# Kernel optimization log

Hardware: AMD Instinct MI355X
Metric: run time of the kernel (lower is better)

The kernel has to match this reference:

```python
import jax, jax.numpy as jnp
import numpy as np

B, S_SRC, S_TGT = 4096, 32, 32
V_SRC, V_TGT, E, H = 96, 128, 128, 512
SOS = 1


def _lstm_cell(h, c, x, Wih, Whh, bih, bhh):
    # PyTorch LSTM gate layout: [i, f, g, o] along 4H
    gates = x @ Wih.T + bih + h @ Whh.T + bhh  # (B, 4H)
    i, f, g, o = jnp.split(gates, 4, axis=-1)
    i, f, o = jax.nn.sigmoid(i), jax.nn.sigmoid(f), jax.nn.sigmoid(o)
    g = jnp.tanh(g)
    c2 = f * c + i * g
    h2 = o * jnp.tanh(c2)
    return h2, c2


def setup_inputs() -> dict:
    key = jax.random.key(0)
    ks = jax.random.split(key, 16)
    u = lambda k, shp, s: jax.random.uniform(k, shp, jnp.float32, -s, s)
    sh = 1.0 / np.sqrt(H)
    emb_src = u(ks[0], (V_SRC, E), 0.1).at[0].set(0.0)  # padding_idx=0
    emb_tgt = u(ks[1], (V_TGT, E), 0.1).at[0].set(0.0)
    inp = {
        "src_seq": jax.random.randint(ks[2], (B, S_SRC), 1, V_SRC),
        "src_lengths": jax.random.randint(ks[3], (B,), 1, S_SRC + 1),
        "tgt_seq": jax.random.randint(ks[4], (B, S_TGT), 1, V_TGT),
        "emb_src": emb_src,
        "enc_Wih": u(ks[5], (4 * H, E), sh),
        "enc_Whh": u(ks[6], (4 * H, H), sh),
        "enc_bih": u(ks[7], (4 * H,), sh),
        "enc_bhh": u(ks[8], (4 * H,), sh),
        "emb_tgt": emb_tgt,
        "dec_Wih": u(ks[9], (4 * H, E), sh),
        "dec_Whh": u(ks[10], (4 * H, H), sh),
        "dec_bih": u(ks[11], (4 * H,), sh),
        "dec_bhh": u(ks[12], (4 * H,), sh),
        "W_out": u(ks[13], (V_TGT, H), sh),
        "b_out": u(ks[14], (V_TGT,), sh),
    }
    return inp


def reference(src_seq, src_lengths, tgt_seq,
              emb_src, enc_Wih, enc_Whh, enc_bih, enc_bhh,
              emb_tgt, dec_Wih, dec_Whh, dec_bih, dec_bhh,
              W_out, b_out):
    batch = src_seq.shape[0]
    h0 = jnp.zeros((batch, H), jnp.float32)
    c0 = jnp.zeros((batch, H), jnp.float32)

    # ---- Encoder: masked LSTM == pack_padded_sequence semantics ----
    x_src = emb_src[src_seq]                                # (B, S, E)
    x_src_t = jnp.swapaxes(x_src, 0, 1)                     # (S, B, E)
    mask = (jnp.arange(S_SRC)[:, None] < src_lengths[None, :])[:, :, None]  # (S,B,1)

    def enc_step(carry, inp):
        h, c = carry
        x, m = inp
        h2, c2 = _lstm_cell(h, c, x, enc_Wih, enc_Whh, enc_bih, enc_bhh)
        h = jnp.where(m, h2, h)
        c = jnp.where(m, c2, c)
        return (h, c), None

    (h_enc, c_enc), _ = jax.lax.scan(enc_step, (h0, c0), (x_src_t, mask))

    # ---- Decoder: full teacher forcing (ratio=1.0), eval-mode dropout ----
    dec_in = jnp.concatenate(
        [jnp.full((batch, 1), SOS, tgt_seq.dtype), tgt_seq[:, :-1]], axis=1)  # (B, T)
    x_tgt_t = jnp.swapaxes(emb_tgt[dec_in], 0, 1)           # (T, B, E)

    def dec_step(carry, x):
        h, c = carry
        h2, c2 = _lstm_cell(h, c, x, dec_Wih, dec_Whh, dec_bih, dec_bhh)
        return (h2, c2), h2

    _, hs = jax.lax.scan(dec_step, (h_enc, c_enc), x_tgt_t)  # (T, B, H)

    logits = jnp.einsum('tbh,vh->btv', hs, W_out) + b_out    # (B, T, V_TGT)
    return logits
```

## Files before the change

### kernel.cpp

```cpp
#include <hip/hip_runtime.h>
#include <hip/hip_bf16.h>
#include <hip/hip_fp16.h>
#include <stdint.h>


#define NB     4096
#define SSRC   32
#define STGT   32
#define NVSRC  96
#define NVTGT  128
#define ED     128
#define HD     512
#define G4     2048
#define NBHD   ((size_t)NB * HD)

typedef __attribute__((ext_vector_type(8))) _Float16 half8;
typedef __attribute__((ext_vector_type(4))) float fx4;

#define AS_G __attribute__((address_space(1)))
#define AS_L __attribute__((address_space(3)))

__device__ __forceinline__ void gl2lds16(const void* g, void* l) {
    __builtin_amdgcn_global_load_lds((const AS_G uint32_t*)g, (AS_L uint32_t*)l, 16, 0, 0);
}

__device__ __forceinline__ float sigf(float x) { return 1.0f / (1.0f + __expf(-x)); }
__device__ __forceinline__ float tanhfast(float x) { return 1.0f - 2.0f / (__expf(2.0f * x) + 1.0f); }

__global__ __launch_bounds__(256) void convert_all(
    const float* __restrict__ s1, int n1, _Float16* __restrict__ d1,
    const float* __restrict__ s2, int n2, _Float16* __restrict__ d2,
    const float* __restrict__ s3, int n3, _Float16* __restrict__ d3)
{
    int i = (int)blockIdx.x * 256 + threadIdx.x;
    if (i < n1) { d1[i] = (_Float16)s1[i]; return; }
    i -= n1;
    if (i < n2) { d2[i] = (_Float16)s2[i]; return; }
    i -= n2;
    if (i < n3) d3[i] = (_Float16)s3[i];
}

__global__ __launch_bounds__(256) void transpose2_f32(
    const float* __restrict__ inA, float* __restrict__ outTA,
    const float* __restrict__ inB, float* __restrict__ outTB)
{
    __shared__ float ls[32][33];
    int bid = (int)blockIdx.x;
    const float* in; float* outT;
    if (bid < 256) { in = inA; outT = outTA; }
    else           { in = inB; outT = outTB; bid -= 256; }
    const int rtiles = G4 / 32;
    const int bx = bid % rtiles;
    const int by = bid / rtiles;
    const int tx = threadIdx.x & 31, ty = threadIdx.x >> 5;
    #pragma unroll
    for (int i = 0; i < 4; i++) {
        int rr = ty + i * 8;
        ls[rr][tx] = in[(size_t)(bx * 32 + rr) * ED + by * 32 + tx];
    }
    __syncthreads();
    #pragma unroll
    for (int i = 0; i < 4; i++) {
        int rr = ty + i * 8;
        outT[(size_t)(by * 32 + rr) * G4 + bx * 32 + tx] = ls[tx][rr];
    }
}

__global__ __launch_bounds__(256) void build_tables2(
    const float* __restrict__ embS, const float* __restrict__ WTS,
    const float* __restrict__ bihS, const float* __restrict__ bhhS,
    float* __restrict__ projS,
    const float* __restrict__ embT, const float* __restrict__ WTT,
    const float* __restrict__ bihT, const float* __restrict__ bhhT,
    float* __restrict__ projT)
{
    __shared__ float embL[8][ED];
    int bid = (int)blockIdx.x;
    const float *emb, *WT, *bih, *bhh; float* proj;
    if (bid < (NVSRC / 8) * 8) { emb = embS; WT = WTS; bih = bihS; bhh = bhhS; proj = projS; }
    else { bid -= (NVSRC / 8) * 8; emb = embT; WT = WTT; bih = bihT; bhh = bhhT; proj = projT; }
    const int gc = bid & 7;
    const int vc = bid >> 3;
    const int g  = gc * 256 + threadIdx.x;
    for (int i = threadIdx.x; i < 8 * ED; i += 256)
        embL[i >> 7][i & (ED - 1)] = emb[(size_t)(vc * 8 + (i >> 7)) * ED + (i & (ED - 1))];
    __syncthreads();
    float acc[8] = {0, 0, 0, 0, 0, 0, 0, 0};
    for (int e = 0; e < ED; e++) {
        float w = WT[(size_t)e * G4 + g];
        #pragma unroll
        for (int v = 0; v < 8; v++) acc[v] += embL[v][e] * w;
    }
    float bb = bih[g] + bhh[g];
    const int gate = g >> 9, hcol = g & (HD - 1);
    #pragma unroll
    for (int v = 0; v < 8; v++)
        proj[(((size_t)(vc * 8 + v) * HD + hcol) << 2) + gate] = acc[v] + bb;
}

__global__ __launch_bounds__(256) void sort_rows(
    const int* __restrict__ lens, int* __restrict__ perm,
    int* __restrict__ lens_s, int* __restrict__ maxlen)
{
    __shared__ int hist[33];
    __shared__ int base[33];
    const int tid = threadIdx.x;
    if (tid < 33) hist[tid] = 0;
    __syncthreads();
    for (int i = tid; i < NB; i += 256) atomicAdd(&hist[lens[i]], 1);
    __syncthreads();
    if (tid == 0) {
        int s = 0;
        for (int l = 1; l <= 32; l++) { base[l] = s; s += hist[l]; }
    }
    __syncthreads();
    for (int i = tid; i < NB; i += 256) {
        int l = lens[i];
        int pos = atomicAdd(&base[l], 1);
        perm[pos] = i;
        lens_s[pos] = l;
    }
    __syncthreads();
    if (tid < 32) maxlen[tid] = lens_s[tid * 128 + 127];
}

__global__ __launch_bounds__(256) void gather_seq2(
    const int* __restrict__ src, const int* __restrict__ tgt,
    const int* __restrict__ perm,
    int* __restrict__ src_s, int* __restrict__ tgt_s)
{
    int i = (int)blockIdx.x * 256 + threadIdx.x;
    int half = i >> 17;
    int k = i & ((NB * 32) - 1);
    int row = k >> 5, t = k & 31;
    if (half == 0) src_s[k] = src[perm[row] * 32 + t];
    else           tgt_s[k] = tgt[perm[row] * 32 + t];
}

__global__ __launch_bounds__(512, 4) void lstm_step(
    const _Float16* __restrict__ h_r, _Float16* __restrict__ h_w,
    float* __restrict__ c_state,
    const float* __restrict__ proj,
    const int* __restrict__ seq_s, const int* __restrict__ lens_s,
    const int* __restrict__ maxlen,
    const _Float16* __restrict__ W,
    _Float16* __restrict__ hfinal,
    const _Float16* __restrict__ Wo, const float* __restrict__ bout,
    const int* __restrict__ perm, float* __restrict__ out,
    int t, int is_enc, int skip_gemm)
{
    __shared__ __align__(16) _Float16 lsA[128 * 64];
    __shared__ __align__(16) _Float16 lsB[128 * 64];
    __shared__ __align__(16) _Float16 lsBo[16 * 64];

    const int tid = threadIdx.x;
    const int lane = tid & 63;
    const int wid  = tid >> 6;
    const int srow = lane >> 3;
    const int skc  = (((lane & 7) ^ srow)) << 3;
    const int wm   = (wid & 3) * 32;
    const int hgrp = (wid >> 2) * 16;
    const int quad = lane >> 4;
    const int l15  = lane & 15;

    const int x = (int)blockIdx.x & 7, j = (int)blockIdx.x >> 3;
    const int mt = (x & 1) * 16 + (j & 15);
    const int m0 = mt * 128;
    const int ct = (x >> 1) * 4 + (j >> 4);
    const int c0 = ct * 32;

    if (is_enc && t >= maxlen[mt]) return;

    const bool po = (!is_enc) && (t > 0) && ((ct & 1) == 0);
    const int vg = ct >> 1;

    const _Float16 *ag[2], *bg[2];
    #pragma unroll
    for (int i = 0; i < 2; i++) {
        int lr = wid * 16 + i * 8 + srow;
        ag[i] = h_r + (size_t)(m0 + lr) * HD + skc;
        int wr = (lr >> 5) * HD + c0 + (lr & 31);
        bg[i] = W + (size_t)wr * HD + skc;
    }
    const _Float16* bo = Wo + (size_t)(vg * 16 + wid * 8 + srow) * HD + skc;

    fx4 acc[2][4];
    #pragma unroll
    for (int i = 0; i < 2; i++)
        #pragma unroll
        for (int jj = 0; jj < 4; jj++)
            acc[i][jj] = fx4{0.f, 0.f, 0.f, 0.f};
    fx4 acc_o = fx4{0.f, 0.f, 0.f, 0.f};

    if (!skip_gemm) {
        for (int k0 = 0; k0 < HD; k0 += 64) {
            __syncthreads();
            #pragma unroll
            for (int i = 0; i < 2; i++) {
                gl2lds16(ag[i] + k0, &lsA[(wid * 16 + i * 8) * 64]);
                gl2lds16(bg[i] + k0, &lsB[(wid * 16 + i * 8) * 64]);
            }
            if (po && wid < 2)
                gl2lds16(bo + k0, &lsBo[(wid * 8) * 64]);
            __syncthreads();
            #pragma unroll
            for (int kk = 0; kk < 64; kk += 32) {
                const int kc = (kk >> 3) + quad;
                half8 af[2], bf[4];
                #pragma unroll
                for (int mf = 0; mf < 2; mf++) {
                    int ar = wm + mf * 16 + l15;
                    int sw = ((kc ^ (ar & 7)) << 3);
                    af[mf] = *(const half8*)&lsA[ar * 64 + sw];
                }
                #pragma unroll
                for (int g = 0; g < 4; g++) {
                    int br = g * 32 + hgrp + l15;
                    int sw = ((kc ^ (br & 7)) << 3);
                    bf[g] = *(const half8*)&lsB[br * 64 + sw];
                }
                #pragma unroll
                for (int mf = 0; mf < 2; mf++)
                    #pragma unroll
                    for (int g = 0; g < 4; g++)
                        acc[mf][g] = __builtin_amdgcn_mfma_f32_16x16x32_f16(af[mf], bf[g], acc[mf][g], 0, 0, 0);
                if (po) {
                    half8 afo = (wid >> 2) ? af[1] : af[0];
                    half8 bfo = *(const half8*)&lsBo[l15 * 64 + ((kc ^ (l15 & 7)) << 3)];
                    acc_o = __builtin_amdgcn_mfma_f32_16x16x32_f16(afo, bfo, acc_o, 0, 0, 0);
                }
            }
        }
    }

    const int hcol = c0 + hgrp + l15;
    #pragma unroll
    for (int mf = 0; mf < 2; mf++) {
        #pragma unroll
        for (int r = 0; r < 4; r++) {
            int row = m0 + wm + mf * 16 + quad * 4 + r;
            int tok = is_enc ? seq_s[row * SSRC + t]
                             : (t == 0 ? 1 : seq_s[row * STGT + t - 1]);
            const fx4 xp = *(const fx4*)&proj[((size_t)tok * HD + hcol) << 2];
            float gi = acc[mf][0][r] + xp[0];
            float gf = acc[mf][1][r] + xp[1];
            float gg = acc[mf][2][r] + xp[2];
            float go = acc[mf][3][r] + xp[3];
            float ii = sigf(gi), ff = sigf(gf), oo = sigf(go);
            float g2 = tanhfast(gg);
            size_t off = (size_t)row * HD + hcol;
            float cold = c_state[off];
            float c2 = ff * cold + ii * g2;
            float h2 = oo * tanhfast(c2);
            bool cwrite = true;
            if (is_enc) {
                int len = lens_s[row];
                if (t >= len) {
                    c2 = cold;
                    cwrite = false;
                    h2 = (float)h_r[off];
                }
                if (t + 1 == len)
                    hfinal[off] = (_Float16)h2;
            }
            if (cwrite) c_state[off] = c2;
            h_w[off] = (_Float16)h2;
        }
    }

    if (po) {
        const int mfo = wid >> 2;
        const int v = vg * 16 + l15;
        const float bo_b = bout[v];
        #pragma unroll
        for (int r = 0; r < 4; r++) {
            int row = m0 + wm + mfo * 16 + quad * 4 + r;
            int orow = perm[row];
            out[((size_t)orow * STGT + (t - 1)) * NVTGT + v] = acc_o[r] + bo_b;
        }
    }
}

__global__ __launch_bounds__(256, 2) void outproj_batch(
    const _Float16* __restrict__ h_slots, int t0,
    const _Float16* __restrict__ Wo, const float* __restrict__ bout,
    const int* __restrict__ perm,
    float* __restrict__ out)
{
    __shared__ __align__(16) _Float16 lsA[128 * 64];
    __shared__ __align__(16) _Float16 lsB[128 * 64];

    const int tid = threadIdx.x;
    const int lane = tid & 63;
    const int wid  = tid >> 6;
    const int srow = lane >> 3;
    const int skc  = (((lane & 7) ^ srow)) << 3;
    const int wm    = (wid >> 1) * 64;
    const int wncol = wid & 1;
    const int quad  = lane >> 4;
    const int l15   = lane & 15;
    const int bsw   = (l15 & 7);

    const int t  = t0 + ((int)blockIdx.x >> 5);
    const int m0 = ((int)blockIdx.x & 31) * 128;
    const _Float16* h_r = h_slots + (size_t)(t & 15) * NBHD;

    const _Float16 *ag[4], *bg[4];
    #pragma unroll
    for (int i = 0; i < 4; i++) {
        int lr = wid * 32 + i * 8 + srow;
        ag[i] = h_r + (size_t)(m0 + lr) * HD + skc;
        bg[i] = Wo + (size_t)lr * HD + skc;
    }

    fx4 acc[4][4];
    #pragma unroll
    for (int i = 0; i < 4; i++)
        #pragma unroll
        for (int jj = 0; jj < 4; jj++)
            acc[i][jj] = fx4{0.f, 0.f, 0.f, 0.f};

    for (int k0 = 0; k0 < HD; k0 += 64) {
        __syncthreads();
        #pragma unroll
        for (int i = 0; i < 4; i++) {
            int lb = (wid * 32 + i * 8) * 64;
            gl2lds16(ag[i] + k0, &lsA[lb]);
            gl2lds16(bg[i] + k0, &lsB[lb]);
        }
        __syncthreads();
        #pragma unroll
        for (int kk = 0; kk < 64; kk += 32) {
            const int kc = (kk >> 3) + quad;
            const int sw = ((kc ^ bsw) << 3);
            half8 af[4], bf[4];
            #pragma unroll
            for (int mt = 0; mt < 4; mt++)
                af[mt] = *(const half8*)&lsA[(wm + mt * 16 + l15) * 64 + sw];
            #pragma unroll
            for (int nt = 0; nt < 4; nt++)
                bf[nt] = *(const half8*)&lsB[(wncol * 64 + nt * 16 + l15) * 64 + sw];
            #pragma unroll
            for (int mt = 0; mt < 4; mt++)
                #pragma unroll
                for (int nt = 0; nt < 4; nt++)
                    acc[mt][nt] = __builtin_amdgcn_mfma_f32_16x16x32_f16(af[mt], bf[nt], acc[mt][nt], 0, 0, 0);
        }
    }

    #pragma unroll
    for (int mt = 0; mt < 4; mt++)
        #pragma unroll
        for (int nt = 0; nt < 4; nt++) {
            int v = wncol * 64 + nt * 16 + l15;
            float bo = bout[v];
            #pragma unroll
            for (int r = 0; r < 4; r++) {
                int row = m0 + wm + mt * 16 + quad * 4 + r;
                int orow = perm[row];
                out[((size_t)orow * STGT + t) * NVTGT + v] = acc[mt][nt][r] + bo;
            }
        }
}

extern "C" void kernel_launch(void* const* d_in, const int* in_sizes, int n_in,
                              void* d_out, int out_size, void* d_ws, size_t ws_size,
                              hipStream_t stream) {
    (void)in_sizes; (void)n_in; (void)out_size; (void)ws_size;
    const int* src_seq = (const int*)d_in[0];
    const int* src_len = (const int*)d_in[1];
    const int* tgt_seq = (const int*)d_in[2];
    const float* emb_src = (const float*)d_in[3];
    const float* eWih = (const float*)d_in[4];
    const float* eWhh = (const float*)d_in[5];
    const float* ebih = (const float*)d_in[6];
    const float* ebhh = (const float*)d_in[7];
    const float* emb_tgt = (const float*)d_in[8];
    const float* dWih = (const float*)d_in[9];
    const float* dWhh = (const float*)d_in[10];
    const float* dbih = (const float*)d_in[11];
    const float* dbhh = (const float*)d_in[12];
    const float* Wout = (const float*)d_in[13];
    const float* bout = (const float*)d_in[14];
    float* out = (float*)d_out;

    char* ws = (char*)d_ws;
    size_t off = 0;
    auto carve = [&](size_t bytes) { void* p = ws + off; off += (bytes + 255) & ~(size_t)255; return p; };
    float* proj_src = (float*)carve((size_t)NVSRC * G4 * 4);
    float* proj_tgt = (float*)carve((size_t)NVTGT * G4 * 4);
    float* c_state  = (float*)carve(NBHD * 4);
    _Float16* slots = (_Float16*)carve((size_t)18 * NBHD * 2);
    _Float16* eW_h  = (_Float16*)carve((size_t)G4 * HD * 2);
    _Float16* dW_h  = (_Float16*)carve((size_t)G4 * HD * 2);
    _Float16* Wo_h  = (_Float16*)carve((size_t)NVTGT * HD * 2);
    _Float16* hfinal = (_Float16*)carve(NBHD * 2);
    int* perm   = (int*)carve((size_t)NB * 4);
    int* lens_s = (int*)carve((size_t)NB * 4);
    int* maxlen = (int*)carve(32 * 4);
    int* src_s  = (int*)carve((size_t)NB * SSRC * 4);
    int* tgt_s  = (int*)carve((size_t)NB * STGT * 4);
    float* WT_e = (float*)(slots);
    float* WT_d = (float*)((char*)slots + (size_t)ED * G4 * 4);
    auto slot = [&](int i) { return slots + (size_t)i * NBHD; };

    hipMemsetAsync(c_state, 0, NBHD * 4, stream);

    sort_rows<<<dim3(1), dim3(256), 0, stream>>>(src_len, perm, lens_s, maxlen);
    gather_seq2<<<dim3(2 * NB * SSRC / 256), dim3(256), 0, stream>>>(
        src_seq, tgt_seq, perm, src_s, tgt_s);

    {
        int n1 = G4 * HD, n2 = G4 * HD, n3 = NVTGT * HD;
        int nb = (n1 + n2 + n3 + 255) / 256;
        convert_all<<<dim3(nb), dim3(256), 0, stream>>>(
            eWhh, n1, eW_h, dWhh, n2, dW_h, Wout, n3, Wo_h);
    }
    transpose2_f32<<<dim3(512), dim3(256), 0, stream>>>(eWih, WT_e, dWih, WT_d);
    build_tables2<<<dim3((NVSRC / 8) * 8 + (NVTGT / 8) * 8), dim3(256), 0, stream>>>(
        emb_src, WT_e, ebih, ebhh, proj_src,
        emb_tgt, WT_d, dbih, dbhh, proj_tgt);

    for (int s = 0; s < 32; s++) {
        lstm_step<<<dim3(512), dim3(512), 0, stream>>>(
            slot(16 + (s & 1)), slot(16 + ((s + 1) & 1)), c_state,
            proj_src, src_s, lens_s, maxlen, eW_h, hfinal,
            Wo_h, bout, perm, out, s, 1, (s == 0));
    }
    for (int t = 0; t < 32; t++) {
        const _Float16* hr = (t == 0) ? hfinal : slot((t - 1) & 15);
        lstm_step<<<dim3(512), dim3(512), 0, stream>>>(
            hr, slot(t & 15), c_state,
            proj_tgt, tgt_s, lens_s, maxlen, dW_h, hfinal,
            Wo_h, bout, perm, out, t, 0, 0);
    }
    outproj_batch<<<dim3(32), dim3(256), 0, stream>>>(
        slots, 31, Wo_h, bout, perm, out);
}
```

Baseline: 1.374 ms.

## Enlarge LSTM step tiles, double-buffer LDS loads, batch output projection

The per-step LSTM kernel now uses 256-row tiles (256 blocks instead of 512) with a double-buffered LDS pipeline: global-to-LDS prefetch of the next K chunk runs while MFMAs work on the current one, coordinated by explicit vmcnt waits and setprio. The output projection fused into each decoder step is removed, and instead outproj_batch runs every 16 steps over the buffered hidden-state slots. This aims to raise reuse of the weight tile, hide load latency, and cut per-step extra work. In exchange it doubles LDS use and register pressure (occupancy hint drops to 2) and gives fewer blocks per launch.

```diff
diff --git a/kernel.cpp b/kernel.cpp
--- a/kernel.cpp
+++ b/kernel.cpp
@@ -121,7 +121,7 @@
         lens_s[pos] = l;
     }
     __syncthreads();
-    if (tid < 32) maxlen[tid] = lens_s[tid * 128 + 127];
+    if (tid < 16) maxlen[tid] = lens_s[tid * 256 + 255];
 }
 
 __global__ __launch_bounds__(256) void gather_seq2(
@@ -137,7 +137,7 @@
     else           tgt_s[k] = tgt[perm[row] * 32 + t];
 }
 
-__global__ __launch_bounds__(512, 4) void lstm_step(
+__global__ __launch_bounds__(512, 2) void lstm_step(
     const _Float16* __restrict__ h_r, _Float16* __restrict__ h_w,
     float* __restrict__ c_state,
     const float* __restrict__ proj,
@@ -145,97 +145,112 @@
     const int* __restrict__ maxlen,
     const _Float16* __restrict__ W,
     _Float16* __restrict__ hfinal,
-    const _Float16* __restrict__ Wo, const float* __restrict__ bout,
-    const int* __restrict__ perm, float* __restrict__ out,
     int t, int is_enc, int skip_gemm)
 {
-    __shared__ __align__(16) _Float16 lsA[128 * 64];
-    __shared__ __align__(16) _Float16 lsB[128 * 64];
-    __shared__ __align__(16) _Float16 lsBo[16 * 64];
+    __shared__ __align__(16) _Float16 lsA[2][256 * 64];
+    __shared__ __align__(16) _Float16 lsB[2][128 * 64];
 
     const int tid = threadIdx.x;
     const int lane = tid & 63;
     const int wid  = tid >> 6;
     const int srow = lane >> 3;
     const int skc  = (((lane & 7) ^ srow)) << 3;
-    const int wm   = (wid & 3) * 32;
+    const int wm   = (wid & 3) * 64;
     const int hgrp = (wid >> 2) * 16;
     const int quad = lane >> 4;
     const int l15  = lane & 15;
 
     const int x = (int)blockIdx.x & 7, j = (int)blockIdx.x >> 3;
-    const int mt = (x & 1) * 16 + (j & 15);
-    const int m0 = mt * 128;
-    const int ct = (x >> 1) * 4 + (j >> 4);
+    const int mt = (x & 1) * 8 + (j & 7);
+    const int m0 = mt * 256;
+    const int ct = (x >> 1) * 4 + (j >> 3);
     const int c0 = ct * 32;
 
     if (is_enc && t >= maxlen[mt]) return;
 
-    const bool po = (!is_enc) && (t > 0) && ((ct & 1) == 0);
-    const int vg = ct >> 1;
-
-    const _Float16 *ag[2], *bg[2];
+    const _Float16 *ag[4], *bg[2];
+    #pragma unroll
+    for (int i = 0; i < 4; i++) {
+        int lr = wid * 32 + i * 8 + srow;
+        ag[i] = h_r + (size_t)(m0 + lr) * HD + skc;
+    }
     #pragma unroll
     for (int i = 0; i < 2; i++) {
         int lr = wid * 16 + i * 8 + srow;
-        ag[i] = h_r + (size_t)(m0 + lr) * HD + skc;
         int wr = (lr >> 5) * HD + c0 + (lr & 31);
         bg[i] = W + (size_t)wr * HD + skc;
     }
-    const _Float16* bo = Wo + (size_t)(vg * 16 + wid * 8 + srow) * HD + skc;
-
-    fx4 acc[2][4];
-    #pragma unroll
-    for (int i = 0; i < 2; i++)
+
+    fx4 acc[4][4];
+    #pragma unroll
+    for (int i = 0; i < 4; i++)
         #pragma unroll
         for (int jj = 0; jj < 4; jj++)
             acc[i][jj] = fx4{0.f, 0.f, 0.f, 0.f};
-    fx4 acc_o = fx4{0.f, 0.f, 0.f, 0.f};
 
     if (!skip_gemm) {
-        for (int k0 = 0; k0 < HD; k0 += 64) {
-            __syncthreads();
-            #pragma unroll
-            for (int i = 0; i < 2; i++) {
-                gl2lds16(ag[i] + k0, &lsA[(wid * 16 + i * 8) * 64]);
-                gl2lds16(bg[i] + k0, &lsB[(wid * 16 + i * 8) * 64]);
-            }
-            if (po && wid < 2)
-                gl2lds16(bo + k0, &lsBo[(wid * 8) * 64]);
-            __syncthreads();
+        #pragma unroll
+        for (int i = 0; i < 4; i++)
+            gl2lds16(ag[i], &lsA[0][(wid * 32 + i * 8) * 64]);
+        #pragma unroll
+        for (int i = 0; i < 2; i++)
+            gl2lds16(bg[i], &lsB[0][(wid * 16 + i * 8) * 64]);
+        #pragma unroll
+        for (int i = 0; i < 4; i++)
+            gl2lds16(ag[i] + 64, &lsA[1][(wid * 32 + i * 8) * 64]);
+        #pragma unroll
+        for (int i = 0; i < 2; i++)
+            gl2lds16(bg[i] + 64, &lsB[1][(wid * 16 + i * 8) * 64]);
+
+        #pragma unroll
+        for (int it = 0; it < 8; it++) {
+            if (it < 7) asm volatile("s_waitcnt vmcnt(6)" ::: "memory");
+            else        asm volatile("s_waitcnt vmcnt(0)" ::: "memory");
+            __builtin_amdgcn_s_barrier();
+            __builtin_amdgcn_sched_barrier(0);
+            const _Float16* la = lsA[it & 1];
+            const _Float16* lb = lsB[it & 1];
+            __builtin_amdgcn_s_setprio(1);
             #pragma unroll
             for (int kk = 0; kk < 64; kk += 32) {
                 const int kc = (kk >> 3) + quad;
-                half8 af[2], bf[4];
-                #pragma unroll
-                for (int mf = 0; mf < 2; mf++) {
+                half8 af[4], bf[4];
+                #pragma unroll
+                for (int mf = 0; mf < 4; mf++) {
                     int ar = wm + mf * 16 + l15;
                     int sw = ((kc ^ (ar & 7)) << 3);
-                    af[mf] = *(const half8*)&lsA[ar * 64 + sw];
+                    af[mf] = *(const half8*)&la[ar * 64 + sw];
                 }
                 #pragma unroll
                 for (int g = 0; g < 4; g++) {
                     int br = g * 32 + hgrp + l15;
                     int sw = ((kc ^ (br & 7)) << 3);
-                    bf[g] = *(const half8*)&lsB[br * 64 + sw];
+                    bf[g] = *(const half8*)&lb[br * 64 + sw];
                 }
                 #pragma unroll
-                for (int mf = 0; mf < 2; mf++)
+                for (int mf = 0; mf < 4; mf++)
                     #pragma unroll
                     for (int g = 0; g < 4; g++)
-                        acc[mf][g] = __builtin_amdgcn_mfma_f32_16x16x32_f16(af[mf], bf[g], acc[mf][g], 0, 0, 0);
-                if (po) {
-                    half8 afo = (wid >> 2) ? af[1] : af[0];
-                    half8 bfo = *(const half8*)&lsBo[l15 * 64 + ((kc ^ (l15 & 7)) << 3)];
-                    acc_o = __builtin_amdgcn_mfma_f32_16x16x32_f16(afo, bfo, acc_o, 0, 0, 0);
-                }
+                        acc[mf][g] = __builtin_amdgcn_mfma_f32_16x16x32_f16(
+                            af[mf], bf[g], acc[mf][g], 0, 0, 0);
             }
+            __builtin_amdgcn_s_setprio(0);
+            if (it < 6) {
+                __builtin_amdgcn_sched_barrier(0);
+                __builtin_amdgcn_s_barrier();
+                #pragma unroll
+                for (int i = 0; i < 4; i++)
+                    gl2lds16(ag[i] + (it + 2) * 64, &lsA[it & 1][(wid * 32 + i * 8) * 64]);
+                #pragma unroll
+                for (int i = 0; i < 2; i++)
+                    gl2lds16(bg[i] + (it + 2) * 64, &lsB[it & 1][(wid * 16 + i * 8) * 64]);
+            }
         }
     }
 
     const int hcol = c0 + hgrp + l15;
     #pragma unroll
-    for (int mf = 0; mf < 2; mf++) {
+    for (int mf = 0; mf < 4; mf++) {
         #pragma unroll
         for (int r = 0; r < 4; r++) {
             int row = m0 + wm + mf * 16 + quad * 4 + r;
@@ -267,18 +282,6 @@
             h_w[off] = (_Float16)h2;
         }
     }
-
-    if (po) {
-        const int mfo = wid >> 2;
-        const int v = vg * 16 + l15;
-        const float bo_b = bout[v];
-        #pragma unroll
-        for (int r = 0; r < 4; r++) {
-            int row = m0 + wm + mfo * 16 + quad * 4 + r;
-            int orow = perm[row];
-            out[((size_t)orow * STGT + (t - 1)) * NVTGT + v] = acc_o[r] + bo_b;
-        }
-    }
 }
 
 __global__ __launch_bounds__(256, 2) void outproj_batch(
@@ -422,18 +425,18 @@
         emb_tgt, WT_d, dbih, dbhh, proj_tgt);
 
     for (int s = 0; s < 32; s++) {
-        lstm_step<<<dim3(512), dim3(512), 0, stream>>>(
+        lstm_step<<<dim3(256), dim3(512), 0, stream>>>(
             slot(16 + (s & 1)), slot(16 + ((s + 1) & 1)), c_state,
-            proj_src, src_s, lens_s, maxlen, eW_h, hfinal,
-            Wo_h, bout, perm, out, s, 1, (s == 0));
+            proj_src, src_s, lens_s, maxlen, eW_h, hfinal, s, 1, (s == 0));
     }
     for (int t = 0; t < 32; t++) {
         const _Float16* hr = (t == 0) ? hfinal : slot((t - 1) & 15);
-        lstm_step<<<dim3(512), dim3(512), 0, stream>>>(
+        lstm_step<<<dim3(256), dim3(512), 0, stream>>>(
             hr, slot(t & 15), c_state,
-            proj_tgt, tgt_s, lens_s, maxlen, dW_h, hfinal,
-            Wo_h, bout, perm, out, t, 0, 0);
-    }
-    outproj_batch<<<dim3(32), dim3(256), 0, stream>>>(
-        slots, 31, Wo_h, bout, perm, out);
-}
+            proj_tgt, tgt_s, lens_s, maxlen, dW_h, hfinal, t, 0, 0);
+        if ((t & 15) == 15) {
+            outproj_batch<<<dim3(512), dim3(256), 0, stream>>>(
+                slots, t - 15, Wo_h, bout, perm, out);
+        }
+    }
+}
```

Result: slower. 1.799 ms (+31.0%).

## Unfuse output projection from LSTM step; batch it every 16 steps

Applied to the files above, without the earlier changes.

Removes the output-projection MFMA that ran inside each decoder lstm_step on half the column tiles, and instead launches a separate batched outproj_batch kernel over 16 stored hidden-state slots twice during decoding. The step kernel also skips redundant h writes for encoder rows already past their length, copying h forward only once at t==len. This is meant to cut per-step LDS use, register pressure and load imbalance in the latency-critical recurrent kernel, at the cost of extra launches and a rereading of the hidden states.

```diff
diff --git a/kernel.cpp b/kernel.cpp
--- a/kernel.cpp
+++ b/kernel.cpp
@@ -145,13 +145,10 @@
     const int* __restrict__ maxlen,
     const _Float16* __restrict__ W,
     _Float16* __restrict__ hfinal,
-    const _Float16* __restrict__ Wo, const float* __restrict__ bout,
-    const int* __restrict__ perm, float* __restrict__ out,
     int t, int is_enc, int skip_gemm)
 {
     __shared__ __align__(16) _Float16 lsA[128 * 64];
     __shared__ __align__(16) _Float16 lsB[128 * 64];
-    __shared__ __align__(16) _Float16 lsBo[16 * 64];
 
     const int tid = threadIdx.x;
     const int lane = tid & 63;
@@ -166,13 +163,9 @@
     const int x = (int)blockIdx.x & 7, j = (int)blockIdx.x >> 3;
     const int mt = (x & 1) * 16 + (j & 15);
     const int m0 = mt * 128;
-    const int ct = (x >> 1) * 4 + (j >> 4);
-    const int c0 = ct * 32;
+    const int c0 = ((x >> 1) * 4 + (j >> 4)) * 32;
 
     if (is_enc && t >= maxlen[mt]) return;
-
-    const bool po = (!is_enc) && (t > 0) && ((ct & 1) == 0);
-    const int vg = ct >> 1;
 
     const _Float16 *ag[2], *bg[2];
     #pragma unroll
@@ -182,7 +175,6 @@
         int wr = (lr >> 5) * HD + c0 + (lr & 31);
         bg[i] = W + (size_t)wr * HD + skc;
     }
-    const _Float16* bo = Wo + (size_t)(vg * 16 + wid * 8 + srow) * HD + skc;
 
     fx4 acc[2][4];
     #pragma unroll
@@ -190,7 +182,6 @@
         #pragma unroll
         for (int jj = 0; jj < 4; jj++)
             acc[i][jj] = fx4{0.f, 0.f, 0.f, 0.f};
-    fx4 acc_o = fx4{0.f, 0.f, 0.f, 0.f};
 
     if (!skip_gemm) {
         for (int k0 = 0; k0 < HD; k0 += 64) {
@@ -200,8 +191,6 @@
                 gl2lds16(ag[i] + k0, &lsA[(wid * 16 + i * 8) * 64]);
                 gl2lds16(bg[i] + k0, &lsB[(wid * 16 + i * 8) * 64]);
             }
-            if (po && wid < 2)
-                gl2lds16(bo + k0, &lsBo[(wid * 8) * 64]);
             __syncthreads();
             #pragma unroll
             for (int kk = 0; kk < 64; kk += 32) {
@@ -224,11 +213,6 @@
                     #pragma unroll
                     for (int g = 0; g < 4; g++)
                         acc[mf][g] = __builtin_amdgcn_mfma_f32_16x16x32_f16(af[mf], bf[g], acc[mf][g], 0, 0, 0);
-                if (po) {
-                    half8 afo = (wid >> 2) ? af[1] : af[0];
-                    half8 bfo = *(const half8*)&lsBo[l15 * 64 + ((kc ^ (l15 & 7)) << 3)];
-                    acc_o = __builtin_amdgcn_mfma_f32_16x16x32_f16(afo, bfo, acc_o, 0, 0, 0);
-                }
             }
         }
     }
@@ -252,31 +236,20 @@
             float cold = c_state[off];
             float c2 = ff * cold + ii * g2;
             float h2 = oo * tanhfast(c2);
-            bool cwrite = true;
+            bool cwrite = true, hwrite = true;
             if (is_enc) {
                 int len = lens_s[row];
                 if (t >= len) {
                     c2 = cold;
                     cwrite = false;
-                    h2 = (float)h_r[off];
+                    if (t == len) h2 = (float)h_r[off];
+                    else hwrite = false;
                 }
                 if (t + 1 == len)
                     hfinal[off] = (_Float16)h2;
             }
             if (cwrite) c_state[off] = c2;
-            h_w[off] = (_Float16)h2;
-        }
-    }
-
-    if (po) {
-        const int mfo = wid >> 2;
-        const int v = vg * 16 + l15;
-        const float bo_b = bout[v];
-        #pragma unroll
-        for (int r = 0; r < 4; r++) {
-            int row = m0 + wm + mfo * 16 + quad * 4 + r;
-            int orow = perm[row];
-            out[((size_t)orow * STGT + (t - 1)) * NVTGT + v] = acc_o[r] + bo_b;
+            if (hwrite) h_w[off] = (_Float16)h2;
         }
     }
 }
@@ -424,16 +397,16 @@
     for (int s = 0; s < 32; s++) {
         lstm_step<<<dim3(512), dim3(512), 0, stream>>>(
             slot(16 + (s & 1)), slot(16 + ((s + 1) & 1)), c_state,
-            proj_src, src_s, lens_s, maxlen, eW_h, hfinal,
-            Wo_h, bout, perm, out, s, 1, (s == 0));
+            proj_src, src_s, lens_s, maxlen, eW_h, hfinal, s, 1, (s == 0));
     }
     for (int t = 0; t < 32; t++) {
         const _Float16* hr = (t == 0) ? hfinal : slot((t - 1) & 15);
         lstm_step<<<dim3(512), dim3(512), 0, stream>>>(
             hr, slot(t & 15), c_state,
-            proj_tgt, tgt_s, lens_s, maxlen, dW_h, hfinal,
-            Wo_h, bout, perm, out, t, 0, 0);
-    }
-    outproj_batch<<<dim3(32), dim3(256), 0, stream>>>(
-        slots, 31, Wo_h, bout, perm, out);
-}
+            proj_tgt, tgt_s, lens_s, maxlen, dW_h, hfinal, t, 0, 0);
+        if ((t & 15) == 15) {
+            outproj_batch<<<dim3(512), dim3(256), 0, stream>>>(
+                slots, t - 15, Wo_h, bout, perm, out);
+        }
+    }
+}
```

Result: faster. 1.330 ms (-3.2%).
